# Kernel optimization log

Measured on AMD Instinct MI355X. Metric: run time of the kernel, lower is better.

The kernel has to match this reference:

```python
import jax, jax.numpy as jnp
import numpy as np

B, S, D, H = 2, 2048, 1024, 16
HD = D // H
SCALE = HD ** -0.5

def setup_inputs() -> dict:
    key = jax.random.key(0)
    ks = jax.random.split(key, 5)
    x = jax.random.normal(ks[0], (B, S, D), dtype=jnp.float32)
    Wqkv = jax.random.normal(ks[1], (D, 3 * D), dtype=jnp.float32) * (D ** -0.5)
    bqkv = jnp.zeros((3 * D,), dtype=jnp.float32)
    Wproj = jax.random.normal(ks[2], (D, D), dtype=jnp.float32) * (D ** -0.5)
    bproj = jnp.zeros((D,), dtype=jnp.float32)
    return {"x": x, "Wqkv": Wqkv, "bqkv": bqkv, "Wproj": Wproj, "bproj": bproj}

def reference(x, Wqkv, bqkv, Wproj, bproj):
    b, s, _ = x.shape
    qkv = x @ Wqkv + bqkv                       # [B,S,3D]
    qkv = qkv.reshape(b, s, 3, H, HD)
    q, k, v = [jnp.transpose(qkv[:, :, i], (0, 2, 1, 3)) for i in range(3)]  # [B,H,S,HD]
    attn = jnp.einsum('bhqd,bhkd->bhqk', q, k) * SCALE   # [B,H,S,S]
    attn = jax.nn.softmax(attn, axis=-1)
    out = jnp.einsum('bhqk,bhkd->bhqd', attn, v)         # [B,H,S,HD]
    out = jnp.transpose(out, (0, 2, 1, 3)).reshape(b, s, D)
    return out @ Wproj + bproj
```

## Files before the change

### kernel.cpp

```cpp
#include <hip/hip_runtime.h>
#include <hip/hip_bf16.h>

#define BB 2
#define SS 2048
#define DD 1024
#define HH 16
#define HDD 64
#define MM (BB*SS)
#define NQKV (3*DD)
#define SCALE 0.125f
#define QPRESCALE 0.18033688f

typedef __bf16 bf16_t;
typedef bf16_t bf16x8 __attribute__((ext_vector_type(8)));
typedef float f32x4 __attribute__((ext_vector_type(4)));
typedef float f32x16 __attribute__((ext_vector_type(16)));

__device__ __forceinline__ void gl_lds16(const bf16_t* g, bf16_t* l) {
    __builtin_amdgcn_global_load_lds(
        (const __attribute__((address_space(1))) unsigned int*)(uintptr_t)g,
        (__attribute__((address_space(3))) unsigned int*)(uintptr_t)l,
        16, 0, 0);
}

__global__ __launch_bounds__(256) void convert_f32_bf16(
    const float* __restrict__ src, bf16_t* __restrict__ dst, int n)
{
    int i = (blockIdx.x * 256 + threadIdx.x) * 8;
    if (i < n) {
        float4 a = *(const float4*)(src + i);
        float4 b = *(const float4*)(src + i + 4);
        bf16x8 v;
        v[0]=(bf16_t)a.x; v[1]=(bf16_t)a.y; v[2]=(bf16_t)a.z; v[3]=(bf16_t)a.w;
        v[4]=(bf16_t)b.x; v[5]=(bf16_t)b.y; v[6]=(bf16_t)b.z; v[7]=(bf16_t)b.w;
        *reinterpret_cast<bf16x8*>(dst + i) = v;
    }
}

__global__ __launch_bounds__(256) void transpose_f32_bf16(
    const float* __restrict__ src, bf16_t* __restrict__ dst, int R, int C)
{
    __shared__ float tile[32][33];
    const int tx = threadIdx.x & 31, ty = threadIdx.x >> 5;
    const int r0 = blockIdx.y * 32, c0 = blockIdx.x * 32;
    #pragma unroll
    for (int i = 0; i < 32; i += 8)
        tile[ty + i][tx] = src[(size_t)(r0 + ty + i) * C + c0 + tx];
    __syncthreads();
    #pragma unroll
    for (int i = 0; i < 32; i += 8)
        dst[(size_t)(c0 + ty + i) * R + r0 + tx] = (bf16_t)tile[tx][ty + i];
}

template <int MODE>
__global__ __launch_bounds__(256) void gemm_bt(
    const bf16_t* __restrict__ A, const bf16_t* __restrict__ Bt,
    const float* __restrict__ bias, float* __restrict__ outf,
    bf16_t* __restrict__ qw, bf16_t* __restrict__ kw, bf16_t* __restrict__ vtw,
    int N, int K)
{
    __shared__ __align__(16) bf16_t As[128 * 32];
    __shared__ __align__(16) bf16_t Bs[128 * 32];

    const int tid  = threadIdx.x;
    const int w    = tid >> 6;
    const int lane = tid & 63;
    const int lr   = lane & 15;
    const int quad = lane >> 4;
    const int m0   = blockIdx.y * 128;
    const int n0   = blockIdx.x * 128;
    const int wm   = w >> 1;
    const int wn   = w & 1;

    f32x4 acc[4][4];
    #pragma unroll
    for (int i = 0; i < 4; i++)
        #pragma unroll
        for (int j = 0; j < 4; j++) acc[i][j] = (f32x4){0.f, 0.f, 0.f, 0.f};

    const int stgRow = lane >> 2;
    const int stgCol = (lane & 3) * 8;
    const bf16_t* aPtr = A  + (size_t)(m0 + w * 32 + stgRow) * K + stgCol;
    const bf16_t* bPtr = Bt + (size_t)(n0 + w * 32 + stgRow) * K + stgCol;
    bf16_t* aDst = As + w * 1024;
    bf16_t* bDst = Bs + w * 1024;
    const size_t rowSkip = (size_t)16 * K;

    for (int ks = 0; ks < K; ks += 32) {
        __syncthreads();
        gl_lds16(aPtr + ks,           aDst);
        gl_lds16(aPtr + rowSkip + ks, aDst + 512);
        gl_lds16(bPtr + ks,           bDst);
        gl_lds16(bPtr + rowSkip + ks, bDst + 512);
        __syncthreads();

        bf16x8 af[4], bf[4];
        #pragma unroll
        for (int mi = 0; mi < 4; mi++)
            af[mi] = *reinterpret_cast<const bf16x8*>(&As[(wm * 64 + mi * 16 + lr) * 32 + quad * 8]);
        #pragma unroll
        for (int ni = 0; ni < 4; ni++)
            bf[ni] = *reinterpret_cast<const bf16x8*>(&Bs[(wn * 64 + ni * 16 + lr) * 32 + quad * 8]);
        #pragma unroll
        for (int mi = 0; mi < 4; mi++)
            #pragma unroll
            for (int ni = 0; ni < 4; ni++)
                acc[mi][ni] = __builtin_amdgcn_mfma_f32_16x16x32_bf16(af[mi], bf[ni], acc[mi][ni], 0, 0, 0);
    }

    #pragma unroll
    for (int mi = 0; mi < 4; mi++) {
        #pragma unroll
        for (int ni = 0; ni < 4; ni++) {
            #pragma unroll
            for (int reg = 0; reg < 4; reg++) {
                int row = m0 + wm * 64 + mi * 16 + quad * 4 + reg;
                int col = n0 + wn * 64 + ni * 16 + lr;
                float val = acc[mi][ni][reg] + bias[col];
                if constexpr (MODE == 0) {
                    int b = row >> 11, s = row & 2047;
                    int which = col >> 10, d = col & 1023;
                    int h = d >> 6, hd = d & 63;
                    size_t bh = (size_t)(b * HH + h);
                    if (which == 0)      qw[(bh * SS + s) * HDD + hd] = (bf16_t)(val * QPRESCALE);
                    else if (which == 1) kw[(bh * SS + s) * HDD + hd] = (bf16_t)val;
                    else                 vtw[(bh * HDD + hd) * SS + s] = (bf16_t)val;
                } else {
                    outf[(size_t)row * N + col] = val;
                }
            }
        }
    }
}

__global__ __launch_bounds__(512, 4) void attn_kernel(
    const bf16_t* __restrict__ qws, const bf16_t* __restrict__ kws,
    const bf16_t* __restrict__ vtws, bf16_t* __restrict__ ob)
{
    __shared__ __align__(16) bf16_t smem[33536];
    bf16_t* Ks  = smem;
    bf16_t* Vts = smem + 8320;
    bf16_t* Pb  = smem + 16640;

    const int tid  = threadIdx.x;
    const int w    = tid >> 6;
    const int g    = w >> 2;
    const int wg   = w & 3;
    const int lane = tid & 63;
    const int ln31 = lane & 31;
    const int ln5  = lane >> 5;

    const int qb = blockIdx.x;
    const int bh = blockIdx.y;
    const int b  = bh >> 4;
    const int h  = bh & 15;

    const bf16_t* Qh  = qws  + (size_t)bh * SS * HDD;
    const bf16_t* Kh  = kws  + (size_t)bh * SS * HDD;
    const bf16_t* Vth = vtws + (size_t)bh * HDD * SS;

    const int q0w    = qb * 128 + wg * 32;
    const int kvbase = g * 1024;
    const int kofs   = g * 520;

    bf16x8 aq[4];
    #pragma unroll
    for (int f = 0; f < 4; f++)
        aq[f] = *(const bf16x8*)(Qh + (size_t)(q0w + ln31) * HDD + f * 16 + ln5 * 8);

    const int gtid = tid & 255;
    const int sc = gtid & 7;
    const int sr = gtid >> 3;

    {
        bf16x8 k0 = *(const bf16x8*)(Kh  + (size_t)(kvbase + sr     ) * HDD + sc * 8);
        bf16x8 k1 = *(const bf16x8*)(Kh  + (size_t)(kvbase + sr + 32) * HDD + sc * 8);
        bf16x8 v0 = *(const bf16x8*)(Vth + (size_t)(sr     ) * SS + kvbase + sc * 8);
        bf16x8 v1 = *(const bf16x8*)(Vth + (size_t)(sr + 32) * SS + kvbase + sc * 8);
        *reinterpret_cast<bf16x8*>(&Ks [(kofs + sc * 65 + sr     ) * 8]) = k0;
        *reinterpret_cast<bf16x8*>(&Ks [(kofs + sc * 65 + sr + 32) * 8]) = k1;
        *reinterpret_cast<bf16x8*>(&Vts[(kofs + sc * 65 + sr     ) * 8]) = v0;
        *reinterpret_cast<bf16x8*>(&Vts[(kofs + sc * 65 + sr + 32) * 8]) = v1;
    }
    __syncthreads();

    float l[16];
    f32x16 o[2];
    #pragma unroll
    for (int r = 0; r < 16; r++) l[r] = 0.f;
    #pragma unroll
    for (int ni = 0; ni < 2; ni++)
        #pragma unroll
        for (int r = 0; r < 16; r++) o[ni][r] = 0.f;

    for (int it = 0; it < 16; ++it) {
        f32x16 sfr[2];
        #pragma unroll
        for (int ni = 0; ni < 2; ni++) {
            #pragma unroll
            for (int r = 0; r < 16; r++) sfr[ni][r] = 0.f;
            #pragma unroll
            for (int f = 0; f < 4; f++) {
                bf16x8 kb = *reinterpret_cast<const bf16x8*>(
                    &Ks[(kofs + (2 * f + ln5) * 65 + ni * 32 + ln31) * 8]);
                sfr[ni] = __builtin_amdgcn_mfma_f32_32x32x16_bf16(aq[f], kb, sfr[ni], 0, 0, 0);
            }
        }

        bf16x8 nk0, nk1, nv0, nv1;
        const bool more = (it + 1 < 16);
        if (more) {
            const int kvn = kvbase + (it + 1) * 64;
            nk0 = *(const bf16x8*)(Kh  + (size_t)(kvn + sr     ) * HDD + sc * 8);
            nk1 = *(const bf16x8*)(Kh  + (size_t)(kvn + sr + 32) * HDD + sc * 8);
            nv0 = *(const bf16x8*)(Vth + (size_t)(sr     ) * SS + kvn + sc * 8);
            nv1 = *(const bf16x8*)(Vth + (size_t)(sr + 32) * SS + kvn + sc * 8);
        }

        float p[2][16];
        #pragma unroll
        for (int ni = 0; ni < 2; ni++)
            #pragma unroll
            for (int r = 0; r < 16; r++)
                p[ni][r] = __builtin_amdgcn_exp2f(sfr[ni][r]);
        #pragma unroll
        for (int r = 0; r < 16; r++)
            l[r] += p[0][r] + p[1][r];

        {
            const int cbase  = (ln31 >> 3);
            const int within = lane & 7;
            #pragma unroll
            for (int ni = 0; ni < 2; ni++) {
                const int c = ni * 4 + cbase;
                #pragma unroll
                for (int r = 0; r < 16; r++) {
                    const int q = (r & 3) + 8 * (r >> 2) + 4 * ln5;
                    Pb[(w * 264 + c * 33 + q) * 8 + within] = (bf16_t)p[ni][r];
                }
            }
        }

        bf16x8 ap[4];
        #pragma unroll
        for (int f = 0; f < 4; f++)
            ap[f] = *reinterpret_cast<const bf16x8*>(
                &Pb[(w * 264 + (2 * f + ln5) * 33 + ln31) * 8]);

        #pragma unroll
        for (int ni = 0; ni < 2; ni++) {
            #pragma unroll
            for (int f = 0; f < 4; f++) {
                bf16x8 vb = *reinterpret_cast<const bf16x8*>(
                    &Vts[(kofs + (2 * f + ln5) * 65 + ni * 32 + ln31) * 8]);
                o[ni] = __builtin_amdgcn_mfma_f32_32x32x16_bf16(ap[f], vb, o[ni], 0, 0, 0);
            }
        }

        if (more) {
            __syncthreads();
            *reinterpret_cast<bf16x8*>(&Ks [(kofs + sc * 65 + sr     ) * 8]) = nk0;
            *reinterpret_cast<bf16x8*>(&Ks [(kofs + sc * 65 + sr + 32) * 8]) = nk1;
            *reinterpret_cast<bf16x8*>(&Vts[(kofs + sc * 65 + sr     ) * 8]) = nv0;
            *reinterpret_cast<bf16x8*>(&Vts[(kofs + sc * 65 + sr + 32) * 8]) = nv1;
            __syncthreads();
        }
    }

    #pragma unroll
    for (int off = 1; off < 32; off <<= 1)
        #pragma unroll
        for (int r = 0; r < 16; r++)
            l[r] += __shfl_xor(l[r], off, 64);

    __syncthreads();
    float* Of = (float*)smem;
    float* Lf = (float*)(smem + 16640);
    if (g == 1) {
        #pragma unroll
        for (int ni = 0; ni < 2; ni++) {
            #pragma unroll
            for (int r = 0; r < 16; r++) {
                const int q = (r & 3) + 8 * (r >> 2) + 4 * ln5;
                Of[(wg * 32 + q) * 64 + ni * 32 + ln31] = o[ni][r];
            }
        }
        if (ln31 == 0) {
            #pragma unroll
            for (int r = 0; r < 16; r++) {
                const int q = (r & 3) + 8 * (r >> 2) + 4 * ln5;
                Lf[wg * 32 + q] = l[r];
            }
        }
    }
    __syncthreads();
    if (g == 0) {
        float inv[16];
        #pragma unroll
        for (int r = 0; r < 16; r++) {
            const int q = (r & 3) + 8 * (r >> 2) + 4 * ln5;
            inv[r] = 1.f / (l[r] + Lf[wg * 32 + q]);
        }
        #pragma unroll
        for (int ni = 0; ni < 2; ni++) {
            #pragma unroll
            for (int r = 0; r < 16; r++) {
                const int q  = (r & 3) + 8 * (r >> 2) + 4 * ln5;
                const int hd = ni * 32 + ln31;
                float val = (o[ni][r] + Of[(wg * 32 + q) * 64 + hd]) * inv[r];
                ob[((size_t)b * SS + q0w + q) * DD + h * HDD + hd] = (bf16_t)val;
            }
        }
    }
}

extern "C" void kernel_launch(void* const* d_in, const int* in_sizes, int n_in,
                              void* d_out, int out_size, void* d_ws, size_t ws_size,
                              hipStream_t stream) {
    const float* x     = (const float*)d_in[0];
    const float* Wqkv  = (const float*)d_in[1];
    const float* bqkv  = (const float*)d_in[2];
    const float* Wproj = (const float*)d_in[3];
    const float* bproj = (const float*)d_in[4];
    float* out = (float*)d_out;

    const size_t NEL = (size_t)MM * DD;
    bf16_t* qws    = (bf16_t*)d_ws;
    bf16_t* kws    = qws  + NEL;
    bf16_t* vtws   = kws  + NEL;
    bf16_t* xb     = vtws + NEL;
    bf16_t* ows    = xb;
    bf16_t* wqkvt  = xb + NEL;
    bf16_t* wprojt = wqkvt + (size_t)NQKV * DD;

    convert_f32_bf16<<<(int)(NEL / 8 / 256), 256, 0, stream>>>(x, xb, (int)NEL);
    transpose_f32_bf16<<<dim3(NQKV / 32, DD / 32), 256, 0, stream>>>(Wqkv, wqkvt, DD, NQKV);
    transpose_f32_bf16<<<dim3(DD / 32, DD / 32), 256, 0, stream>>>(Wproj, wprojt, DD, DD);

    gemm_bt<0><<<dim3(NQKV / 128, MM / 128), 256, 0, stream>>>(
        xb, wqkvt, bqkv, nullptr, qws, kws, vtws, NQKV, DD);

    attn_kernel<<<dim3(SS / 128, BB * HH), 512, 0, stream>>>(qws, kws, vtws, ows);

    gemm_bt<1><<<dim3(DD / 128, MM / 128), 256, 0, stream>>>(
        ows, wprojt, bproj, out, nullptr, nullptr, nullptr, DD, DD);
}
```

Before: 211.9 us.

## Keep P in registers via transposed S MFMA, merge transposes, smaller proj GEMM tile

The attention kernel now computes S transposed (K as the A operand), so the exp'd P fragments can feed the PV MFMA straight from registers. This removes the per-iteration LDS round-trip for P and shrinks the row-sum bookkeeping to a scalar. V is stored in a padded row layout for that operand pattern, which needs split 4-element LDS stores and loads. In addition, the two weight transposes are merged into one launch, and the output projection uses a 64-row tile GEMM to launch more blocks.

```diff
diff --git a/kernel.cpp b/kernel.cpp
--- a/kernel.cpp
+++ b/kernel.cpp
@@ -12,6 +12,7 @@
 #define QPRESCALE 0.18033688f
 
 typedef __bf16 bf16_t;
+typedef bf16_t bf16x4 __attribute__((ext_vector_type(4)));
 typedef bf16_t bf16x8 __attribute__((ext_vector_type(8)));
 typedef float f32x4 __attribute__((ext_vector_type(4)));
 typedef float f32x16 __attribute__((ext_vector_type(16)));
@@ -37,12 +38,18 @@
     }
 }
 
-__global__ __launch_bounds__(256) void transpose_f32_bf16(
-    const float* __restrict__ src, bf16_t* __restrict__ dst, int R, int C)
+__global__ __launch_bounds__(256) void transpose2_f32_bf16(
+    const float* __restrict__ Wqkv, const float* __restrict__ Wproj,
+    bf16_t* __restrict__ wqkvt, bf16_t* __restrict__ wprojt)
 {
     __shared__ float tile[32][33];
+    const int bx = blockIdx.x;
+    const float* src; bf16_t* dst; int C, bxl;
+    if (bx < 96) { src = Wqkv;  dst = wqkvt;  C = NQKV; bxl = bx; }
+    else         { src = Wproj; dst = wprojt; C = DD;   bxl = bx - 96; }
+    const int R = DD;
     const int tx = threadIdx.x & 31, ty = threadIdx.x >> 5;
-    const int r0 = blockIdx.y * 32, c0 = blockIdx.x * 32;
+    const int r0 = blockIdx.y * 32, c0 = bxl * 32;
     #pragma unroll
     for (int i = 0; i < 32; i += 8)
         tile[ty + i][tx] = src[(size_t)(r0 + ty + i) * C + c0 + tx];
@@ -133,14 +140,77 @@
     }
 }
 
+__global__ __launch_bounds__(256) void gemm_bt64(
+    const bf16_t* __restrict__ A, const bf16_t* __restrict__ Bt,
+    const float* __restrict__ bias, float* __restrict__ outf, int N, int K)
+{
+    __shared__ __align__(16) bf16_t As[64 * 32];
+    __shared__ __align__(16) bf16_t Bs[128 * 32];
+
+    const int tid  = threadIdx.x;
+    const int w    = tid >> 6;
+    const int lane = tid & 63;
+    const int lr   = lane & 15;
+    const int quad = lane >> 4;
+    const int m0   = blockIdx.y * 64;
+    const int n0   = blockIdx.x * 128;
+    const int wm   = w >> 1;
+    const int wn   = w & 1;
+
+    f32x4 acc[2][4];
+    #pragma unroll
+    for (int i = 0; i < 2; i++)
+        #pragma unroll
+        for (int j = 0; j < 4; j++) acc[i][j] = (f32x4){0.f, 0.f, 0.f, 0.f};
+
+    const int stgRow = lane >> 2;
+    const int stgCol = (lane & 3) * 8;
+    const bf16_t* aPtr = A  + (size_t)(m0 + w * 16 + stgRow) * K + stgCol;
+    const bf16_t* bPtr = Bt + (size_t)(n0 + w * 32 + stgRow) * K + stgCol;
+    bf16_t* aDst = As + w * 512;
+    bf16_t* bDst = Bs + w * 1024;
+    const size_t rowSkip = (size_t)16 * K;
+
+    for (int ks = 0; ks < K; ks += 32) {
+        __syncthreads();
+        gl_lds16(aPtr + ks,           aDst);
+        gl_lds16(bPtr + ks,           bDst);
+        gl_lds16(bPtr + rowSkip + ks, bDst + 512);
+        __syncthreads();
+
+        bf16x8 af[2], bf[4];
+        #pragma unroll
+        for (int mi = 0; mi < 2; mi++)
+            af[mi] = *reinterpret_cast<const bf16x8*>(&As[(wm * 32 + mi * 16 + lr) * 32 + quad * 8]);
+        #pragma unroll
+        for (int ni = 0; ni < 4; ni++)
+            bf[ni] = *reinterpret_cast<const bf16x8*>(&Bs[(wn * 64 + ni * 16 + lr) * 32 + quad * 8]);
+        #pragma unroll
+        for (int mi = 0; mi < 2; mi++)
+            #pragma unroll
+            for (int ni = 0; ni < 4; ni++)
+                acc[mi][ni] = __builtin_amdgcn_mfma_f32_16x16x32_bf16(af[mi], bf[ni], acc[mi][ni], 0, 0, 0);
+    }
+
+    #pragma unroll
+    for (int mi = 0; mi < 2; mi++)
+        #pragma unroll
+        for (int ni = 0; ni < 4; ni++)
+            #pragma unroll
+            for (int reg = 0; reg < 4; reg++) {
+                int row = m0 + wm * 32 + mi * 16 + quad * 4 + reg;
+                int col = n0 + wn * 64 + ni * 16 + lr;
+                outf[(size_t)row * N + col] = acc[mi][ni][reg] + bias[col];
+            }
+}
+
 __global__ __launch_bounds__(512, 4) void attn_kernel(
     const bf16_t* __restrict__ qws, const bf16_t* __restrict__ kws,
     const bf16_t* __restrict__ vtws, bf16_t* __restrict__ ob)
 {
-    __shared__ __align__(16) bf16_t smem[33536];
-    bf16_t* Ks  = smem;
-    bf16_t* Vts = smem + 8320;
-    bf16_t* Pb  = smem + 16640;
+    __shared__ __align__(16) bf16_t smem[17024];
+    bf16_t* Ks = smem;
+    bf16_t* Vs = smem + 8320;
 
     const int tid  = threadIdx.x;
     const int w    = tid >> 6;
@@ -162,6 +232,7 @@
     const int q0w    = qb * 128 + wg * 32;
     const int kvbase = g * 1024;
     const int kofs   = g * 520;
+    const int vofs   = g * 4352;
 
     bf16x8 aq[4];
     #pragma unroll
@@ -177,21 +248,23 @@
         bf16x8 k1 = *(const bf16x8*)(Kh  + (size_t)(kvbase + sr + 32) * HDD + sc * 8);
         bf16x8 v0 = *(const bf16x8*)(Vth + (size_t)(sr     ) * SS + kvbase + sc * 8);
         bf16x8 v1 = *(const bf16x8*)(Vth + (size_t)(sr + 32) * SS + kvbase + sc * 8);
-        *reinterpret_cast<bf16x8*>(&Ks [(kofs + sc * 65 + sr     ) * 8]) = k0;
-        *reinterpret_cast<bf16x8*>(&Ks [(kofs + sc * 65 + sr + 32) * 8]) = k1;
-        *reinterpret_cast<bf16x8*>(&Vts[(kofs + sc * 65 + sr     ) * 8]) = v0;
-        *reinterpret_cast<bf16x8*>(&Vts[(kofs + sc * 65 + sr + 32) * 8]) = v1;
+        *reinterpret_cast<bf16x8*>(&Ks[(kofs + sc * 65 + sr     ) * 8]) = k0;
+        *reinterpret_cast<bf16x8*>(&Ks[(kofs + sc * 65 + sr + 32) * 8]) = k1;
+        bf16_t* vd0 = &Vs[vofs + (sr     ) * 68 + sc * 8];
+        bf16_t* vd1 = &Vs[vofs + (sr + 32) * 68 + sc * 8];
+        *reinterpret_cast<bf16x4*>(vd0)     = __builtin_shufflevector(v0, v0, 0,1,2,3);
+        *reinterpret_cast<bf16x4*>(vd0 + 4) = __builtin_shufflevector(v0, v0, 4,5,6,7);
+        *reinterpret_cast<bf16x4*>(vd1)     = __builtin_shufflevector(v1, v1, 0,1,2,3);
+        *reinterpret_cast<bf16x4*>(vd1 + 4) = __builtin_shufflevector(v1, v1, 4,5,6,7);
     }
     __syncthreads();
 
-    float l[16];
+    float l = 0.f;
     f32x16 o[2];
     #pragma unroll
-    for (int r = 0; r < 16; r++) l[r] = 0.f;
-    #pragma unroll
-    for (int ni = 0; ni < 2; ni++)
-        #pragma unroll
-        for (int r = 0; r < 16; r++) o[ni][r] = 0.f;
+    for (int nh = 0; nh < 2; nh++)
+        #pragma unroll
+        for (int r = 0; r < 16; r++) o[nh][r] = 0.f;
 
     for (int it = 0; it < 16; ++it) {
         f32x16 sfr[2];
@@ -203,7 +276,7 @@
             for (int f = 0; f < 4; f++) {
                 bf16x8 kb = *reinterpret_cast<const bf16x8*>(
                     &Ks[(kofs + (2 * f + ln5) * 65 + ni * 32 + ln31) * 8]);
-                sfr[ni] = __builtin_amdgcn_mfma_f32_32x32x16_bf16(aq[f], kb, sfr[ni], 0, 0, 0);
+                sfr[ni] = __builtin_amdgcn_mfma_f32_32x32x16_bf16(kb, aq[f], sfr[ni], 0, 0, 0);
             }
         }
 
@@ -221,77 +294,58 @@
         #pragma unroll
         for (int ni = 0; ni < 2; ni++)
             #pragma unroll
-            for (int r = 0; r < 16; r++)
+            for (int r = 0; r < 16; r++) {
                 p[ni][r] = __builtin_amdgcn_exp2f(sfr[ni][r]);
-        #pragma unroll
-        for (int r = 0; r < 16; r++)
-            l[r] += p[0][r] + p[1][r];
-
-        {
-            const int cbase  = (ln31 >> 3);
-            const int within = lane & 7;
-            #pragma unroll
-            for (int ni = 0; ni < 2; ni++) {
-                const int c = ni * 4 + cbase;
-                #pragma unroll
-                for (int r = 0; r < 16; r++) {
-                    const int q = (r & 3) + 8 * (r >> 2) + 4 * ln5;
-                    Pb[(w * 264 + c * 33 + q) * 8 + within] = (bf16_t)p[ni][r];
-                }
-            }
-        }
+                l += p[ni][r];
+            }
 
         bf16x8 ap[4];
         #pragma unroll
-        for (int f = 0; f < 4; f++)
-            ap[f] = *reinterpret_cast<const bf16x8*>(
-                &Pb[(w * 264 + (2 * f + ln5) * 33 + ln31) * 8]);
-
-        #pragma unroll
-        for (int ni = 0; ni < 2; ni++) {
-            #pragma unroll
-            for (int f = 0; f < 4; f++) {
-                bf16x8 vb = *reinterpret_cast<const bf16x8*>(
-                    &Vts[(kofs + (2 * f + ln5) * 65 + ni * 32 + ln31) * 8]);
-                o[ni] = __builtin_amdgcn_mfma_f32_32x32x16_bf16(ap[f], vb, o[ni], 0, 0, 0);
+        for (int c16 = 0; c16 < 4; c16++)
+            #pragma unroll
+            for (int j = 0; j < 8; j++)
+                ap[c16][j] = (bf16_t)p[c16 >> 1][(c16 & 1) * 8 + j];
+
+        #pragma unroll
+        for (int nh = 0; nh < 2; nh++) {
+            const bf16_t* vrow = &Vs[vofs + (nh * 32 + ln31) * 68];
+            #pragma unroll
+            for (int c16 = 0; c16 < 4; c16++) {
+                bf16x4 lo = *(const bf16x4*)(vrow + c16 * 16 + 4 * ln5);
+                bf16x4 hi = *(const bf16x4*)(vrow + c16 * 16 + 8 + 4 * ln5);
+                bf16x8 vb = __builtin_shufflevector(lo, hi, 0, 1, 2, 3, 4, 5, 6, 7);
+                o[nh] = __builtin_amdgcn_mfma_f32_32x32x16_bf16(ap[c16], vb, o[nh], 0, 0, 0);
             }
         }
 
         if (more) {
             __syncthreads();
-            *reinterpret_cast<bf16x8*>(&Ks [(kofs + sc * 65 + sr     ) * 8]) = nk0;
-            *reinterpret_cast<bf16x8*>(&Ks [(kofs + sc * 65 + sr + 32) * 8]) = nk1;
-            *reinterpret_cast<bf16x8*>(&Vts[(kofs + sc * 65 + sr     ) * 8]) = nv0;
-            *reinterpret_cast<bf16x8*>(&Vts[(kofs + sc * 65 + sr + 32) * 8]) = nv1;
+            *reinterpret_cast<bf16x8*>(&Ks[(kofs + sc * 65 + sr     ) * 8]) = nk0;
+            *reinterpret_cast<bf16x8*>(&Ks[(kofs + sc * 65 + sr + 32) * 8]) = nk1;
+            bf16_t* vd0 = &Vs[vofs + (sr     ) * 68 + sc * 8];
+            bf16_t* vd1 = &Vs[vofs + (sr + 32) * 68 + sc * 8];
+            *reinterpret_cast<bf16x4*>(vd0)     = __builtin_shufflevector(nv0, nv0, 0,1,2,3);
+            *reinterpret_cast<bf16x4*>(vd0 + 4) = __builtin_shufflevector(nv0, nv0, 4,5,6,7);
+            *reinterpret_cast<bf16x4*>(vd1)     = __builtin_shufflevector(nv1, nv1, 0,1,2,3);
+            *reinterpret_cast<bf16x4*>(vd1 + 4) = __builtin_shufflevector(nv1, nv1, 4,5,6,7);
             __syncthreads();
         }
     }
 
-    #pragma unroll
-    for (int off = 1; off < 32; off <<= 1)
-        #pragma unroll
-        for (int r = 0; r < 16; r++)
-            l[r] += __shfl_xor(l[r], off, 64);
+    l += __shfl_xor(l, 32, 64);
 
     __syncthreads();
     float* Of = (float*)smem;
-    float* Lf = (float*)(smem + 16640);
+    float* Lf = (float*)(smem + 16384);
+    if (ln5 == 0) Lf[g * 128 + wg * 32 + ln31] = l;
     if (g == 1) {
         #pragma unroll
-        for (int ni = 0; ni < 2; ni++) {
+        for (int nh = 0; nh < 2; nh++)
             #pragma unroll
             for (int r = 0; r < 16; r++) {
                 const int q = (r & 3) + 8 * (r >> 2) + 4 * ln5;
-                Of[(wg * 32 + q) * 64 + ni * 32 + ln31] = o[ni][r];
-            }
-        }
-        if (ln31 == 0) {
-            #pragma unroll
-            for (int r = 0; r < 16; r++) {
-                const int q = (r & 3) + 8 * (r >> 2) + 4 * ln5;
-                Lf[wg * 32 + q] = l[r];
-            }
-        }
+                Of[(wg * 32 + q) * 64 + nh * 32 + ln31] = o[nh][r];
+            }
     }
     __syncthreads();
     if (g == 0) {
@@ -299,18 +353,17 @@
         #pragma unroll
         for (int r = 0; r < 16; r++) {
             const int q = (r & 3) + 8 * (r >> 2) + 4 * ln5;
-            inv[r] = 1.f / (l[r] + Lf[wg * 32 + q]);
-        }
-        #pragma unroll
-        for (int ni = 0; ni < 2; ni++) {
+            inv[r] = 1.f / (Lf[wg * 32 + q] + Lf[128 + wg * 32 + q]);
+        }
+        #pragma unroll
+        for (int nh = 0; nh < 2; nh++)
             #pragma unroll
             for (int r = 0; r < 16; r++) {
                 const int q  = (r & 3) + 8 * (r >> 2) + 4 * ln5;
-                const int hd = ni * 32 + ln31;
-                float val = (o[ni][r] + Of[(wg * 32 + q) * 64 + hd]) * inv[r];
+                const int hd = nh * 32 + ln31;
+                float val = (o[nh][r] + Of[(wg * 32 + q) * 64 + hd]) * inv[r];
                 ob[((size_t)b * SS + q0w + q) * DD + h * HDD + hd] = (bf16_t)val;
             }
-        }
     }
 }
 
@@ -334,14 +387,13 @@
     bf16_t* wprojt = wqkvt + (size_t)NQKV * DD;
 
     convert_f32_bf16<<<(int)(NEL / 8 / 256), 256, 0, stream>>>(x, xb, (int)NEL);
-    transpose_f32_bf16<<<dim3(NQKV / 32, DD / 32), 256, 0, stream>>>(Wqkv, wqkvt, DD, NQKV);
-    transpose_f32_bf16<<<dim3(DD / 32, DD / 32), 256, 0, stream>>>(Wproj, wprojt, DD, DD);
+    transpose2_f32_bf16<<<dim3(128, 32), 256, 0, stream>>>(Wqkv, Wproj, wqkvt, wprojt);
 
     gemm_bt<0><<<dim3(NQKV / 128, MM / 128), 256, 0, stream>>>(
         xb, wqkvt, bqkv, nullptr, qws, kws, vtws, NQKV, DD);
 
     attn_kernel<<<dim3(SS / 128, BB * HH), 512, 0, stream>>>(qws, kws, vtws, ows);
 
-    gemm_bt<1><<<dim3(DD / 128, MM / 128), 256, 0, stream>>>(
-        ows, wprojt, bproj, out, nullptr, nullptr, nullptr, DD, DD);
-}
+    gemm_bt64<<<dim3(DD / 128, MM / 64), 256, 0, stream>>>(
+        ows, wprojt, bproj, out, DD, DD);
+}
```

Measured after the change: 195.4 us. -7.8%, faster.
